# Kernel optimization log

Measured on AMD Instinct MI355X. Metric: run time of the kernel, lower is better.

## Reference

```python
import jax, jax.numpy as jnp
import numpy as np
from jax import lax

B, C, H, W = 4, 512, 32, 32
HEADS, HC, GROUPS = 8, 64, 4
GC = C // GROUPS          # group channels = 128
GH = HEADS // GROUPS      # heads per group = 2
KK = 5                    # offset conv kernel (stage_idx=2)
OFFSET_RANGE_FACTOR = 2.0
LN_EPS = 1e-5


def conv1x1(x, w, b):
    # x: [B,Cin,H,W], w: [Cout,Cin], b: [Cout]
    return jnp.einsum('bchw,oc->bohw', x, w) + b[None, :, None, None]


def ref_points(h, w, n, dtype=jnp.float32):
    # torch linspace(0.5, h-0.5, h) normalized to (-1,1); stacked (y,x)
    ry = ((jnp.arange(h, dtype=dtype) + 0.5) / h) * 2.0 - 1.0
    rx = ((jnp.arange(w, dtype=dtype) + 0.5) / w) * 2.0 - 1.0
    ref = jnp.stack(jnp.meshgrid(ry, rx, indexing='ij'), axis=-1)  # [h,w,2]
    return jnp.broadcast_to(ref[None], (n, h, w, 2))


def grid_sample(img, grid):
    # F.grid_sample: bilinear, align_corners=True, padding_mode='zeros'
    # img: [N,C,Hs,Ws], grid: [N,*S,2] with grid[...,0]=x, grid[...,1]=y in [-1,1]
    N, Cc, Hs, Ws = img.shape
    gx = (grid[..., 0] + 1.0) * 0.5 * (Ws - 1)
    gy = (grid[..., 1] + 1.0) * 0.5 * (Hs - 1)
    x0 = jnp.floor(gx)
    y0 = jnp.floor(gy)
    wx1 = gx - x0
    wy1 = gy - y0
    imgf = img.reshape(N, Cc, Hs * Ws)

    def corner(ix, iy, wgt):
        valid = ((ix >= 0) & (ix <= Ws - 1) & (iy >= 0) & (iy <= Hs - 1)).astype(img.dtype)
        flat = (jnp.clip(iy, 0, Hs - 1) * Ws + jnp.clip(ix, 0, Ws - 1)).astype(jnp.int32)
        vals = jax.vmap(lambda im, f: im[:, f])(imgf, flat)  # [N,C,*S]
        return vals * (wgt * valid)[:, None]

    return (corner(x0, y0, (1 - wx1) * (1 - wy1))
            + corner(x0 + 1, y0, wx1 * (1 - wy1))
            + corner(x0, y0 + 1, (1 - wx1) * wy1)
            + corner(x0 + 1, y0 + 1, wx1 * wy1))


def setup_inputs() -> dict:
    key = jax.random.key(0)
    ks = jax.random.split(key, 10)

    def w(k, shape, s=0.02):
        return jax.random.normal(k, shape, jnp.float32) * s

    return {
        'x': jax.random.normal(ks[0], (B, C, H, W), jnp.float32),
        'w_q': w(ks[1], (C, C)), 'b_q': jnp.zeros((C,), jnp.float32),
        'w_k': w(ks[2], (C, C)), 'b_k': jnp.zeros((C,), jnp.float32),
        'w_v': w(ks[3], (C, C)), 'b_v': jnp.zeros((C,), jnp.float32),
        'w_o': w(ks[4], (C, C)), 'b_o': jnp.zeros((C,), jnp.float32),
        'dw_w': w(ks[5], (GC, 1, KK, KK), 0.05),  # depthwise offset conv
        'dw_b': jnp.zeros((GC,), jnp.float32),
        'ln_g': jnp.ones((GC,), jnp.float32),
        'ln_b': jnp.zeros((GC,), jnp.float32),
        'off_w': w(ks[6], (2, GC), 0.05),          # 1x1 conv -> 2 offset channels
        'rpe': w(ks[7], (HEADS, 2 * H - 1, 2 * W - 1), 0.01),
    }


def reference(x, w_q, b_q, w_k, b_k, w_v, b_v, w_o, b_o,
              dw_w, dw_b, ln_g, ln_b, off_w, rpe):
    q = conv1x1(x, w_q, b_q)
    # 'b (g c) h w -> (b g) c h w'
    q_off = q.reshape(B * GROUPS, GC, H, W)
    # depthwise conv kk=5, stride=1, pad=2
    off = lax.conv_general_dilated(q_off, dw_w, (1, 1),
                                   ((KK // 2, KK // 2), (KK // 2, KK // 2)),
                                   dimension_numbers=('NCHW', 'OIHW', 'NCHW'),
                                   feature_group_count=GC) + dw_b[None, :, None, None]
    # LayerNormProxy over channel dim
    mu = jnp.mean(off, axis=1, keepdims=True)
    var = jnp.mean((off - mu) ** 2, axis=1, keepdims=True)
    off = (off - mu) * lax.rsqrt(var + LN_EPS) * ln_g[None, :, None, None] + ln_b[None, :, None, None]
    off = jax.nn.gelu(off, approximate=False)
    off = jnp.einsum('bchw,oc->bohw', off, off_w)  # [B*G, 2, Hk, Wk] (y,x channels)
    Hk, Wk = off.shape[2], off.shape[3]
    nS = Hk * Wk
    off_range = jnp.array([1.0 / Hk, 1.0 / Wk], dtype=x.dtype).reshape(1, 2, 1, 1)
    off = jnp.tanh(off) * off_range * OFFSET_RANGE_FACTOR
    off = jnp.transpose(off, (0, 2, 3, 1))  # [B*G, Hk, Wk, 2]
    ref = ref_points(Hk, Wk, B * GROUPS, x.dtype)
    pos = off + ref  # offset_range_factor >= 0 branch
    # deformable sampling (grid takes (x,y))
    xs = grid_sample(x.reshape(B * GROUPS, GC, H, W), pos[..., ::-1])  # [B*G,GC,Hk,Wk]
    xs = xs.reshape(B, C, 1, nS)
    qf = q.reshape(B * HEADS, HC, H * W)
    k = conv1x1(xs, w_k, b_k).reshape(B * HEADS, HC, nS)
    v = conv1x1(xs, w_v, b_v).reshape(B * HEADS, HC, nS)
    attn = jnp.einsum('bcm,bcn->bmn', qf, k) * (HC ** -0.5)  # [B*Hd, HW, nS]
    # continuous relative-position bias via bilinear table lookup
    rpe_b = jnp.broadcast_to(rpe[None], (B,) + rpe.shape).reshape(
        B * GROUPS, GH, rpe.shape[1], rpe.shape[2])
    q_grid = ref_points(H, W, B * GROUPS, x.dtype)
    disp = (q_grid.reshape(B * GROUPS, H * W, 1, 2)
            - pos.reshape(B * GROUPS, 1, nS, 2)) * 0.5  # [B*G, HW, nS, 2]
    bias = grid_sample(rpe_b, disp[..., ::-1]).reshape(B * HEADS, H * W, nS)
    attn = jax.nn.softmax(attn + bias, axis=2)
    out = jnp.einsum('bmn,bcn->bcm', attn, v).reshape(B, C, H, W)
    y = conv1x1(out, w_o, b_o)
    return (y,
            pos.reshape(B, GROUPS, Hk, Wk, 2),
            ref.reshape(B, GROUPS, Hk, Wk, 2))
```

## Files before the change

kernel.cpp:

```cpp
#include <hip/hip_runtime.h>
#include <hip/hip_bf16.h>

typedef __hip_bfloat16 bf16;
typedef __attribute__((ext_vector_type(8))) short bf16x8;
typedef __attribute__((ext_vector_type(4))) float f32x4;

#define BDIM 4
#define CDIM 512
#define NHEADS 8
#define NGROUPS 4
#define GCH 128

__device__ __forceinline__ float bf2f(bf16 v) { return __bfloat162float(v); }
__device__ __forceinline__ float bfu2f(unsigned short u) {
  return __uint_as_float(((unsigned)u) << 16);
}
__device__ __forceinline__ unsigned short f2bu(float v) {
  return __hip_bfloat16_raw(__float2bfloat16(v)).x;
}
__device__ __forceinline__ unsigned pack2(float lo, float hi) {
  return (unsigned)f2bu(lo) | ((unsigned)f2bu(hi) << 16);
}

template <bool IN_F32, typename OutT, int NMAT>
__global__ __launch_bounds__(256) void gemm_kernel(
    const float* __restrict__ W0, const float* __restrict__ bias0,
    const float* __restrict__ W1, const float* __restrict__ bias1,
    const void* __restrict__ in,
    OutT* __restrict__ out0, OutT* __restrict__ out1) {
  __shared__ __align__(16) unsigned char smem[8192 * (NMAT + 1)];
  unsigned char* b_lds = smem + 8192 * NMAT;
  const int b = blockIdx.z;
  const int o0 = blockIdx.y * 64;
  const int n0 = blockIdx.x * 64;
  const int t = threadIdx.x, l = t & 63, w = t >> 6;
  const int rg = l >> 4, cl = l & 15;
  const int o_base = (w >> 1) * 32, n_base = (w & 1) * 32;
  const int ao = t >> 2;
  const int ac8 = (t & 3) * 8;
  const int kc2 = (t & 31) * 2;
  const int kn8 = (t >> 5) * 8;
  const unsigned swo = (unsigned)((ao & 7) << 4);
  const float* Ws[2] = {W0, W1};
  const float* Bs[2] = {bias0, bias1};
  OutT* Os[2] = {out0, out1};

  f32x4 acc[NMAT][2][2];
#pragma unroll
  for (int m = 0; m < NMAT; m++)
#pragma unroll
    for (int i = 0; i < 2; i++)
#pragma unroll
      for (int j = 0; j < 2; j++) acc[m][i][j] = {0.f, 0.f, 0.f, 0.f};

  for (int k0 = 0; k0 < 512; k0 += 64) {
#pragma unroll
    for (int m = 0; m < NMAT; m++) {
      const float* wr = Ws[m] + (size_t)(o0 + ao) * 512 + k0;
      const float4 a0 = *(const float4*)(wr + ac8);
      const float4 a1 = *(const float4*)(wr + ac8 + 4);
      const float4 c0 = *(const float4*)(wr + ac8 + 32);
      const float4 c1 = *(const float4*)(wr + ac8 + 36);
      uint4 ua = {pack2(a0.x, a0.y), pack2(a0.z, a0.w),
                  pack2(a1.x, a1.y), pack2(a1.z, a1.w)};
      uint4 ub = {pack2(c0.x, c0.y), pack2(c0.z, c0.w),
                  pack2(c1.x, c1.y), pack2(c1.z, c1.w)};
      unsigned char* am = smem + 8192 * m;
      *(uint4*)(am + ao * 128 + ((2 * ac8) ^ swo)) = ua;
      *(uint4*)(am + ao * 128 + ((2 * ac8 + 64) ^ swo)) = ub;
    }
    if constexpr (IN_F32) {
      const float* inb = (const float*)in + (size_t)b * 524288;
      const float* p0 = inb + (size_t)(k0 + kc2) * 1024 + n0 + kn8;
      union { float4 v[2]; float f[8]; } r0, r1;
      r0.v[0] = *(const float4*)p0;
      r0.v[1] = *(const float4*)(p0 + 4);
      r1.v[0] = *(const float4*)(p0 + 1024);
      r1.v[1] = *(const float4*)(p0 + 1028);
#pragma unroll
      for (int i = 0; i < 8; i++) {
        const int n = kn8 + i;
        *(unsigned*)(b_lds + n * 128 + ((2 * kc2) ^ ((n & 7) << 4))) =
            pack2(r0.f[i], r1.f[i]);
      }
    } else {
      const unsigned short* inb = (const unsigned short*)in + (size_t)b * 524288;
      union { uint4 v; unsigned short hw[8]; } r0, r1;
      r0.v = *(const uint4*)(inb + (size_t)(k0 + kc2) * 1024 + n0 + kn8);
      r1.v = *(const uint4*)(inb + (size_t)(k0 + kc2 + 1) * 1024 + n0 + kn8);
#pragma unroll
      for (int i = 0; i < 8; i++) {
        const int n = kn8 + i;
        const unsigned v32 = (unsigned)r0.hw[i] | ((unsigned)r1.hw[i] << 16);
        *(unsigned*)(b_lds + n * 128 + ((2 * kc2) ^ ((n & 7) << 4))) = v32;
      }
    }
    __syncthreads();
#pragma unroll
    for (int kk = 0; kk < 2; kk++) {
      bf16x8 bfr[2];
#pragma unroll
      for (int nn = 0; nn < 2; nn++) {
        const int n_loc = n_base + 16 * nn + cl;
        bfr[nn] = *(const bf16x8*)(b_lds + n_loc * 128 +
                                   ((64 * kk + 16 * rg) ^ ((n_loc & 7) << 4)));
      }
#pragma unroll
      for (int m = 0; m < NMAT; m++) {
        bf16x8 af[2];
#pragma unroll
        for (int mi = 0; mi < 2; mi++) {
          const int o_loc = o_base + 16 * mi + cl;
          af[mi] = *(const bf16x8*)(smem + 8192 * m + o_loc * 128 +
                                    ((64 * kk + 16 * rg) ^ ((o_loc & 7) << 4)));
        }
#pragma unroll
        for (int mi = 0; mi < 2; mi++)
#pragma unroll
          for (int nn = 0; nn < 2; nn++)
            acc[m][mi][nn] = __builtin_amdgcn_mfma_f32_16x16x32_bf16(
                af[mi], bfr[nn], acc[m][mi][nn], 0, 0, 0);
      }
    }
    __syncthreads();
  }

  float* o_st = (float*)smem;
#pragma unroll
  for (int m = 0; m < NMAT; m++) {
    __syncthreads();
#pragma unroll
    for (int mi = 0; mi < 2; mi++)
#pragma unroll
      for (int nn = 0; nn < 2; nn++)
#pragma unroll
        for (int r = 0; r < 4; r++)
          o_st[(o_base + 16 * mi + 4 * rg + r) * 64 + n_base + 16 * nn + cl] =
              acc[m][mi][nn][r];
    __syncthreads();
    const int eo = t >> 4;
    const int en = (t & 15) * 4;
#pragma unroll
    for (int pass = 0; pass < 4; pass++) {
      const int o_loc = eo + pass * 16;
      const f32x4 v = *(const f32x4*)(o_st + o_loc * 64 + en);
      const float bv = Bs[m][o0 + o_loc];
      if constexpr (sizeof(OutT) == 2) {
        ushort4 u;
        u.x = f2bu(v[0] + bv);
        u.y = f2bu(v[1] + bv);
        u.z = f2bu(v[2] + bv);
        u.w = f2bu(v[3] + bv);
        *(ushort4*)((bf16*)Os[m] + ((size_t)b * 512 + o0 + o_loc) * 1024 + n0 + en) = u;
      } else {
        float4 r = {v[0] + bv, v[1] + bv, v[2] + bv, v[3] + bv};
        *(float4*)((float*)Os[m] + ((size_t)b * 512 + o0 + o_loc) * 1024 + n0 + en) = r;
      }
    }
  }
}

__global__ __launch_bounds__(512) void offset_kernel(
    const bf16* __restrict__ q, const float* __restrict__ dw_w,
    const float* __restrict__ dw_b, const float* __restrict__ ln_g,
    const float* __restrict__ ln_b, const float* __restrict__ off_w,
    float* __restrict__ pos, float* __restrict__ out_pos, float* __restrict__ out_ref) {
  __shared__ unsigned short q_s[5][36][128];
  __shared__ float red_a[4][2][2];
  __shared__ float red_p[4][2][2];
  const int bg = blockIdx.x;
  const int h = blockIdx.y;
  const int b = bg >> 2, g = bg & 3;
  const int t = threadIdx.x;

  for (int task = t; task < 640; task += 512) {
    const int ky = task >> 7, c = task & 127;
    const int y = h + ky - 2;
    if (y >= 0 && y < 32) {
      const unsigned short* qrow =
          (const unsigned short*)q + ((size_t)b * CDIM + g * GCH + c) * 1024 + y * 32;
      q_s[ky][0][c] = 0;
      q_s[ky][1][c] = 0;
#pragma unroll
      for (int x8 = 0; x8 < 4; x8++) {
        union { uint4 u; unsigned short s[8]; } vv;
        vv.u = *(const uint4*)(qrow + x8 * 8);
#pragma unroll
        for (int i = 0; i < 8; i++) q_s[ky][2 + x8 * 8 + i][c] = vv.s[i];
      }
      q_s[ky][34][c] = 0;
      q_s[ky][35][c] = 0;
    } else {
#pragma unroll
      for (int xi = 0; xi < 36; xi++) q_s[ky][xi][c] = 0;
    }
  }

  const int wslot = t >> 7;
  const int c = t & 127;
  const int half = c >> 6;
  const int lane = t & 63;
  float wgt[25];
#pragma unroll
  for (int i = 0; i < 25; i++) wgt[i] = dw_w[c * 25 + i];
  const float cbias = dw_b[c];
  const float gam = ln_g[c], bet = ln_b[c];
  const float ow0 = off_w[c], ow1 = off_w[GCH + c];
  __syncthreads();

  for (int j = 0; j < 8; j++) {
    const int w = wslot * 8 + j;
    float s = cbias;
#pragma unroll
    for (int ky = 0; ky < 5; ky++)
#pragma unroll
      for (int kx = 0; kx < 5; kx++)
        s += wgt[ky * 5 + kx] * bfu2f(q_s[ky][w + kx][c]);
    float ssum = s, ssq = s * s;
#pragma unroll
    for (int o = 1; o < 64; o <<= 1) {
      ssum += __shfl_xor(ssum, o);
      ssq += __shfl_xor(ssq, o);
    }
    if (lane == 0) { red_a[wslot][half][0] = ssum; red_a[wslot][half][1] = ssq; }
    __syncthreads();
    const float mu = (red_a[wslot][0][0] + red_a[wslot][1][0]) * (1.0f / 128.0f);
    const float var = (red_a[wslot][0][1] + red_a[wslot][1][1]) * (1.0f / 128.0f) - mu * mu;
    const float xn = (s - mu) * rsqrtf(var + 1e-5f) * gam + bet;
    const float ge = 0.5f * xn * (1.0f + erff(xn * 0.70710678118654752f));
    float p0 = ow0 * ge, p1 = ow1 * ge;
#pragma unroll
    for (int o = 1; o < 64; o <<= 1) {
      p0 += __shfl_xor(p0, o);
      p1 += __shfl_xor(p1, o);
    }
    if (lane == 0) { red_p[wslot][half][0] = p0; red_p[wslot][half][1] = p1; }
    __syncthreads();
    if (c == 0) {
      const float oy = tanhf(red_p[wslot][0][0] + red_p[wslot][1][0]) * 0.0625f;
      const float ox = tanhf(red_p[wslot][0][1] + red_p[wslot][1][1]) * 0.0625f;
      const float ry = ((float)h + 0.5f) * (2.0f / 32.0f) - 1.0f;
      const float rx = ((float)w + 0.5f) * (2.0f / 32.0f) - 1.0f;
      const float py = oy + ry, px = ox + rx;
      const size_t idx = (size_t)bg * 1024 + h * 32 + w;
      pos[idx * 2] = py;
      pos[idx * 2 + 1] = px;
      out_pos[idx * 2] = py;
      out_pos[idx * 2 + 1] = px;
      out_ref[idx * 2] = ry;
      out_ref[idx * 2 + 1] = rx;
    }
  }
}

__global__ __launch_bounds__(256) void sample_kernel(
    const float* __restrict__ x, const float* __restrict__ pos, bf16* __restrict__ xs) {
  const int bg = blockIdx.x, c = blockIdx.y;
  const int b = bg >> 2, g = bg & 3;
  __shared__ float plane[1024];
  const float* xp = x + ((size_t)b * CDIM + g * GCH + c) * 1024;
  for (int i = threadIdx.x; i < 1024; i += 256) plane[i] = xp[i];
  __syncthreads();
  for (int s = threadIdx.x; s < 1024; s += 256) {
    const float py = pos[((size_t)bg * 1024 + s) * 2];
    const float px = pos[((size_t)bg * 1024 + s) * 2 + 1];
    const float gx = (px + 1.0f) * 15.5f;
    const float gy = (py + 1.0f) * 15.5f;
    const float x0f = floorf(gx), y0f = floorf(gy);
    const float wx = gx - x0f, wy = gy - y0f;
    const int ix = (int)x0f, iy = (int)y0f;
    float r = 0.0f;
    const bool vx0 = (ix >= 0) & (ix <= 31), vx1 = (ix + 1 >= 0) & (ix + 1 <= 31);
    const bool vy0 = (iy >= 0) & (iy <= 31), vy1 = (iy + 1 >= 0) & (iy + 1 <= 31);
    if (vy0 && vx0) r += plane[iy * 32 + ix] * (1.0f - wx) * (1.0f - wy);
    if (vy0 && vx1) r += plane[iy * 32 + ix + 1] * wx * (1.0f - wy);
    if (vy1 && vx0) r += plane[(iy + 1) * 32 + ix] * (1.0f - wx) * wy;
    if (vy1 && vx1) r += plane[(iy + 1) * 32 + ix + 1] * wx * wy;
    xs[((size_t)bg * GCH + c) * 1024 + s] = __float2bfloat16(r);
  }
}

__global__ __launch_bounds__(512) void attn_kernel(
    const bf16* __restrict__ q, const bf16* __restrict__ kk,
    const bf16* __restrict__ vv, const float* __restrict__ pos,
    const float* __restrict__ rpe, bf16* __restrict__ ao) {
  __shared__ __align__(16) unsigned char smem[51976];
  float* rpe_f = (float*)(smem + 32768);
  float* m_x = (float*)(smem + 50952);
  float* s_x = (float*)(smem + 51464);

  const int bh = blockIdx.y;
  const int m0 = blockIdx.x * 64;
  const int b = bh >> 3, h = bh & 7;
  const int g = h >> 1;
  const int bg = b * 4 + g;
  const int t = threadIdx.x, l = t & 63, w = t >> 6;
  const int wq = w & 3, half = w >> 2;
  const int rg = l >> 4, cl = l & 15;
  const int t2 = t & 255;
  const size_t hbase = ((size_t)b * CDIM + h * 64) * 1024;
  const unsigned short* qu = (const unsigned short*)q;

  unsigned char* k_base = smem + half * 8192;
  unsigned char* v_base = smem + 16384 + half * 8192;
  float* pos_a = (float*)(smem + 49928) + half * 128;

  for (int i = t; i < 65 * 66; i += 512) {
    const int y = i / 66, x = i - y * 66;
    float v = 0.0f;
    if (y >= 1 && y <= 63 && x >= 1 && x <= 63)
      v = rpe[h * 3969 + (y - 1) * 63 + (x - 1)];
    rpe_f[i] = v;
  }

  const int qloc = 16 * wq + cl;
  const int qm = m0 + qloc;
  const float qy15 = 15.5f * (((float)(qm >> 5) + 0.5f) * (2.0f / 32.0f) - 1.0f);
  const float qx15 = 15.5f * (((float)(qm & 31) + 0.5f) * (2.0f / 32.0f) - 1.0f);

  bf16x8 bq[2];
#pragma unroll
  for (int kc = 0; kc < 2; kc++) {
    bf16x8 a;
#pragma unroll
    for (int j = 0; j < 8; j++)
      a[j] = (short)qu[hbase + (size_t)(32 * kc + 8 * rg + j) * 1024 + qm];
    bq[kc] = a;
  }

  float rmax = -1e30f, rsum = 0.0f;
  f32x4 oacc[4] = {{0.f,0.f,0.f,0.f},{0.f,0.f,0.f,0.f},
                   {0.f,0.f,0.f,0.f},{0.f,0.f,0.f,0.f}};

  const float* posb = pos + (size_t)bg * 2048;
  const unsigned swl = (unsigned)((cl & 7) << 4);
  const int kc2 = (t2 & 31) * 2;
  const int kn8 = (t2 >> 5) * 8;
  const int vc = t2 >> 2;
  const int vh = (t2 & 3) * 32;

  for (int tile = 0; tile < 8; tile++) {
    const int n0 = half * 512 + tile * 64;
    {
      union { uint4 v; unsigned short hw[8]; } r0, r1;
      r0.v = *(const uint4*)(kk + hbase + (size_t)kc2 * 1024 + n0 + kn8);
      r1.v = *(const uint4*)(kk + hbase + (size_t)(kc2 + 1) * 1024 + n0 + kn8);
#pragma unroll
      for (int i = 0; i < 8; i++) {
        const int n = kn8 + i;
        const unsigned v32 = (unsigned)r0.hw[i] | ((unsigned)r1.hw[i] << 16);
        *(unsigned*)(k_base + n * 128 + ((kc2 * 2) ^ ((n & 7) << 4))) = v32;
      }
      const uint4 s0 = *(const uint4*)(vv + hbase + (size_t)vc * 1024 + n0 + vh / 2);
      const uint4 s1 = *(const uint4*)(vv + hbase + (size_t)vc * 1024 + n0 + vh / 2 + 8);
      *(uint4*)(v_base + vc * 128 + (vh ^ ((vc & 7) << 4))) = s0;
      *(uint4*)(v_base + vc * 128 + ((vh + 16) ^ ((vc & 7) << 4))) = s1;
      if (t2 < 128) pos_a[t2] = 31.0f - 15.5f * posb[2 * n0 + t2];
    }
    __syncthreads();

    f32x4 sf[4];
#pragma unroll
    for (int tn = 0; tn < 4; tn++) {
      const int nrow = 16 * tn + cl;
      const bf16x8 a0 = *(const bf16x8*)(k_base + nrow * 128 + ((16 * rg) ^ swl));
      const bf16x8 a1 = *(const bf16x8*)(k_base + nrow * 128 + ((64 + 16 * rg) ^ swl));
      f32x4 z = {0.f, 0.f, 0.f, 0.f};
      z = __builtin_amdgcn_mfma_f32_16x16x32_bf16(a0, bq[0], z, 0, 0, 0);
      z = __builtin_amdgcn_mfma_f32_16x16x32_bf16(a1, bq[1], z, 0, 0, 0);
      sf[tn] = z;
    }

#pragma unroll
    for (int tn = 0; tn < 4; tn++)
#pragma unroll
      for (int r = 0; r < 4; r++) {
        const int key = 16 * tn + 4 * rg + r;
        const float gyc = qy15 + pos_a[2 * key];
        const float gxc = qx15 + pos_a[2 * key + 1];
        const float y0f = floorf(gyc), x0f = floorf(gxc);
        const float wy = gyc - y0f, wx = gxc - x0f;
        const int iy1 = (int)y0f + 1, ix1 = (int)x0f + 1;
        const float* tp = rpe_f + iy1 * 66 + ix1;
        const float t00 = tp[0], t01 = tp[1];
        const float t10 = tp[66], t11 = tp[67];
        const float r0v = t00 + (t01 - t00) * wx;
        const float r1v = t10 + (t11 - t10) * wx;
        const float bias = r0v + (r1v - r0v) * wy;
        sf[tn][r] = sf[tn][r] * 0.125f + bias;
      }

    float tmax = sf[0][0];
#pragma unroll
    for (int tn = 0; tn < 4; tn++)
#pragma unroll
      for (int r = 0; r < 4; r++) tmax = fmaxf(tmax, sf[tn][r]);
    tmax = fmaxf(tmax, __shfl_xor(tmax, 16));
    tmax = fmaxf(tmax, __shfl_xor(tmax, 32));
    const float nmax = fmaxf(rmax, tmax);
    const float corr = __expf(rmax - nmax);
    rmax = nmax;
    float lsum = 0.0f;
    unsigned pw[8];
#pragma unroll
    for (int tn = 0; tn < 4; tn++) {
      const float p0 = __expf(sf[tn][0] - nmax);
      const float p1 = __expf(sf[tn][1] - nmax);
      const float p2 = __expf(sf[tn][2] - nmax);
      const float p3 = __expf(sf[tn][3] - nmax);
      lsum += (p0 + p1) + (p2 + p3);
      pw[2 * tn] = pack2(p0, p1);
      pw[2 * tn + 1] = pack2(p2, p3);
    }
    lsum += __shfl_xor(lsum, 16);
    lsum += __shfl_xor(lsum, 32);
    rsum = rsum * corr + lsum;
#pragma unroll
    for (int tc = 0; tc < 4; tc++) {
      oacc[tc][0] *= corr; oacc[tc][1] *= corr;
      oacc[tc][2] *= corr; oacc[tc][3] *= corr;
    }

    __syncthreads();

#pragma unroll
    for (int tn = 0; tn < 4; tn++) {
      *(unsigned*)(k_base + qloc * 128 + ((2 * (16 * tn + 4 * rg)) ^ swl)) = pw[2 * tn];
      *(unsigned*)(k_base + qloc * 128 + ((2 * (16 * tn + 4 * rg) + 4) ^ swl)) = pw[2 * tn + 1];
    }

#pragma unroll
    for (int kc = 0; kc < 2; kc++) {
      const bf16x8 pb = *(const bf16x8*)(k_base + qloc * 128 + ((2 * (32 * kc + 8 * rg)) ^ swl));
#pragma unroll
      for (int tc = 0; tc < 4; tc++) {
        const int crow = 16 * tc + cl;
        const bf16x8 av = *(const bf16x8*)(v_base + crow * 128 + ((2 * (32 * kc + 8 * rg)) ^ swl));
        oacc[tc] = __builtin_amdgcn_mfma_f32_16x16x32_bf16(av, pb, oacc[tc], 0, 0, 0);
      }
    }
    __syncthreads();
  }

  if (l < 16) {
    m_x[half * 64 + wq * 16 + cl] = rmax;
    s_x[half * 64 + wq * 16 + cl] = rsum;
  }
  __syncthreads();
  const float m0v = m_x[wq * 16 + cl], m1v = m_x[64 + wq * 16 + cl];
  const float s0v = s_x[wq * 16 + cl], s1v = s_x[64 + wq * 16 + cl];
  const float M = fmaxf(m0v, m1v);
  const float f0 = __expf(m0v - M), f1 = __expf(m1v - M);
  const float inv = 1.0f / (f0 * s0v + f1 * s1v);
  const float scale = (half == 0 ? f0 : f1) * inv;
  float* o_st = (float*)smem;
  if (half == 0) {
#pragma unroll
    for (int tc = 0; tc < 4; tc++)
#pragma unroll
      for (int r = 0; r < 4; r++)
        o_st[(16 * tc + 4 * rg + r) * 66 + qloc] = oacc[tc][r] * scale;
  }
  __syncthreads();
  if (half == 1) {
#pragma unroll
    for (int tc = 0; tc < 4; tc++)
#pragma unroll
      for (int r = 0; r < 4; r++)
        o_st[(16 * tc + 4 * rg + r) * 66 + qloc] += oacc[tc][r] * scale;
  }
  __syncthreads();
  {
    const int c = t >> 3, mq = (t & 7) * 8;
    unsigned u[4];
#pragma unroll
    for (int i = 0; i < 4; i++)
      u[i] = pack2(o_st[c * 66 + mq + 2 * i], o_st[c * 66 + mq + 2 * i + 1]);
    uint4 outv = {u[0], u[1], u[2], u[3]};
    *(uint4*)(ao + hbase + (size_t)c * 1024 + m0 + mq) = outv;
  }
}

extern "C" void kernel_launch(void* const* d_in, const int* in_sizes, int n_in,
                              void* d_out, int out_size, void* d_ws, size_t ws_size,
                              hipStream_t stream) {
  const float* x    = (const float*)d_in[0];
  const float* w_q  = (const float*)d_in[1];
  const float* b_q  = (const float*)d_in[2];
  const float* w_k  = (const float*)d_in[3];
  const float* b_k  = (const float*)d_in[4];
  const float* w_v  = (const float*)d_in[5];
  const float* b_v  = (const float*)d_in[6];
  const float* w_o  = (const float*)d_in[7];
  const float* b_o  = (const float*)d_in[8];
  const float* dw_w = (const float*)d_in[9];
  const float* dw_b = (const float*)d_in[10];
  const float* ln_g = (const float*)d_in[11];
  const float* ln_b = (const float*)d_in[12];
  const float* off_w= (const float*)d_in[13];
  const float* rpe  = (const float*)d_in[14];

  float* out_y   = (float*)d_out;
  float* out_pos = out_y + 2097152;
  float* out_ref = out_pos + 32768;

  float* pos_ws = (float*)d_ws;
  bf16*  q_ws   = (bf16*)(pos_ws + 32768);
  bf16*  xs_ws  = q_ws + 2097152;
  bf16*  k_ws   = xs_ws + 2097152;
  bf16*  v_ws   = k_ws + 2097152;
  bf16*  ao_ws  = xs_ws;

  gemm_kernel<true, bf16, 1><<<dim3(16, 8, 4), 256, 0, stream>>>(
      w_q, b_q, nullptr, nullptr, x, q_ws, (bf16*)nullptr);
  offset_kernel<<<dim3(16, 32), 512, 0, stream>>>(q_ws, dw_w, dw_b, ln_g, ln_b, off_w,
                                                  pos_ws, out_pos, out_ref);
  sample_kernel<<<dim3(16, 128), 256, 0, stream>>>(x, pos_ws, xs_ws);
  gemm_kernel<false, bf16, 2><<<dim3(16, 8, 4), 256, 0, stream>>>(
      w_k, b_k, w_v, b_v, xs_ws, k_ws, v_ws);
  attn_kernel<<<dim3(16, 32), 512, 0, stream>>>(q_ws, k_ws, v_ws, pos_ws, rpe, ao_ws);
  gemm_kernel<false, float, 1><<<dim3(16, 8, 4), 256, 0, stream>>>(
      w_o, b_o, nullptr, nullptr, ao_ws, out_y, (float*)nullptr);
}
```

Baseline: 112.6 us.

## Split attention key range across four wave groups with 1024-thread blocks

The attention kernel now uses 1024 threads per block and splits the key dimension four ways instead of two. Each quarter processes 4 tiles of 64 keys instead of 8. The four partial softmax states are merged through shared memory, with two partial output buffers summed at the store. The RPE bias table is stored in shared memory as bf16 rather than fp32 so that the doubled K/V staging still fits. This aims to shorten the serial loop per block and raise wave count on the 512-block grid, at the cost of more shared memory, more merge work, and slightly lower precision in the bias.

```diff
diff --git a/kernel.cpp b/kernel.cpp
--- a/kernel.cpp
+++ b/kernel.cpp
@@ -280,14 +280,14 @@
   }
 }
 
-__global__ __launch_bounds__(512) void attn_kernel(
+__global__ __launch_bounds__(1024, 8) void attn_kernel(
     const bf16* __restrict__ q, const bf16* __restrict__ kk,
     const bf16* __restrict__ vv, const float* __restrict__ pos,
     const float* __restrict__ rpe, bf16* __restrict__ ao) {
-  __shared__ __align__(16) unsigned char smem[51976];
-  float* rpe_f = (float*)(smem + 32768);
-  float* m_x = (float*)(smem + 50952);
-  float* s_x = (float*)(smem + 51464);
+  __shared__ __align__(16) unsigned char smem[78216];
+  unsigned short* rpe_s = (unsigned short*)(smem + 65536);
+  float* m_x = (float*)(smem + 76168);
+  float* s_x = (float*)(smem + 77192);
 
   const int bh = blockIdx.y;
   const int m0 = blockIdx.x * 64;
@@ -295,22 +295,22 @@
   const int g = h >> 1;
   const int bg = b * 4 + g;
   const int t = threadIdx.x, l = t & 63, w = t >> 6;
-  const int wq = w & 3, half = w >> 2;
+  const int wq = w & 3, quarter = w >> 2;
   const int rg = l >> 4, cl = l & 15;
   const int t2 = t & 255;
   const size_t hbase = ((size_t)b * CDIM + h * 64) * 1024;
   const unsigned short* qu = (const unsigned short*)q;
 
-  unsigned char* k_base = smem + half * 8192;
-  unsigned char* v_base = smem + 16384 + half * 8192;
-  float* pos_a = (float*)(smem + 49928) + half * 128;
-
-  for (int i = t; i < 65 * 66; i += 512) {
+  unsigned char* k_base = smem + quarter * 8192;
+  unsigned char* v_base = smem + 32768 + quarter * 8192;
+  float* pos_a = (float*)(smem + 74120) + quarter * 128;
+
+  for (int i = t; i < 65 * 66; i += 1024) {
     const int y = i / 66, x = i - y * 66;
-    float v = 0.0f;
+    unsigned short v = 0;
     if (y >= 1 && y <= 63 && x >= 1 && x <= 63)
-      v = rpe[h * 3969 + (y - 1) * 63 + (x - 1)];
-    rpe_f[i] = v;
+      v = f2bu(rpe[h * 3969 + (y - 1) * 63 + (x - 1)]);
+    rpe_s[i] = v;
   }
 
   const int qloc = 16 * wq + cl;
@@ -339,8 +339,8 @@
   const int vc = t2 >> 2;
   const int vh = (t2 & 3) * 32;
 
-  for (int tile = 0; tile < 8; tile++) {
-    const int n0 = half * 512 + tile * 64;
+  for (int tile = 0; tile < 4; tile++) {
+    const int n0 = quarter * 256 + tile * 64;
     {
       union { uint4 v; unsigned short hw[8]; } r0, r1;
       r0.v = *(const uint4*)(kk + hbase + (size_t)kc2 * 1024 + n0 + kn8);
@@ -381,9 +381,9 @@
         const float y0f = floorf(gyc), x0f = floorf(gxc);
         const float wy = gyc - y0f, wx = gxc - x0f;
         const int iy1 = (int)y0f + 1, ix1 = (int)x0f + 1;
-        const float* tp = rpe_f + iy1 * 66 + ix1;
-        const float t00 = tp[0], t01 = tp[1];
-        const float t10 = tp[66], t11 = tp[67];
+        const unsigned short* tp = rpe_s + iy1 * 66 + ix1;
+        const float t00 = bfu2f(tp[0]), t01 = bfu2f(tp[1]);
+        const float t10 = bfu2f(tp[66]), t11 = bfu2f(tp[67]);
         const float r0v = t00 + (t01 - t00) * wx;
         const float r1v = t10 + (t11 - t10) * wx;
         const float bias = r0v + (r1v - r0v) * wy;
@@ -443,41 +443,50 @@
   }
 
   if (l < 16) {
-    m_x[half * 64 + wq * 16 + cl] = rmax;
-    s_x[half * 64 + wq * 16 + cl] = rsum;
+    m_x[quarter * 64 + qloc] = rmax;
+    s_x[quarter * 64 + qloc] = rsum;
   }
   __syncthreads();
-  const float m0v = m_x[wq * 16 + cl], m1v = m_x[64 + wq * 16 + cl];
-  const float s0v = s_x[wq * 16 + cl], s1v = s_x[64 + wq * 16 + cl];
-  const float M = fmaxf(m0v, m1v);
-  const float f0 = __expf(m0v - M), f1 = __expf(m1v - M);
-  const float inv = 1.0f / (f0 * s0v + f1 * s1v);
-  const float scale = (half == 0 ? f0 : f1) * inv;
-  float* o_st = (float*)smem;
-  if (half == 0) {
+  float mq4[4], sq4[4];
+#pragma unroll
+  for (int qq = 0; qq < 4; qq++) {
+    mq4[qq] = m_x[qq * 64 + qloc];
+    sq4[qq] = s_x[qq * 64 + qloc];
+  }
+  const float M = fmaxf(fmaxf(mq4[0], mq4[1]), fmaxf(mq4[2], mq4[3]));
+  const float e0 = __expf(mq4[0] - M), e1 = __expf(mq4[1] - M);
+  const float e2 = __expf(mq4[2] - M), e3 = __expf(mq4[3] - M);
+  const float inv = 1.0f / (e0 * sq4[0] + e1 * sq4[1] + e2 * sq4[2] + e3 * sq4[3]);
+  const float eq[4] = {e0, e1, e2, e3};
+  const float scale = eq[quarter] * inv;
+  float* o_stA = (float*)smem;
+  float* o_stB = (float*)(smem + 20480);
+  float* mine = (quarter & 1) ? o_stB : o_stA;
+  if (quarter < 2) {
 #pragma unroll
     for (int tc = 0; tc < 4; tc++)
 #pragma unroll
       for (int r = 0; r < 4; r++)
-        o_st[(16 * tc + 4 * rg + r) * 66 + qloc] = oacc[tc][r] * scale;
+        mine[(16 * tc + 4 * rg + r) * 66 + qloc] = oacc[tc][r] * scale;
   }
   __syncthreads();
-  if (half == 1) {
+  if (quarter >= 2) {
 #pragma unroll
     for (int tc = 0; tc < 4; tc++)
 #pragma unroll
       for (int r = 0; r < 4; r++)
-        o_st[(16 * tc + 4 * rg + r) * 66 + qloc] += oacc[tc][r] * scale;
+        mine[(16 * tc + 4 * rg + r) * 66 + qloc] += oacc[tc][r] * scale;
   }
   __syncthreads();
   {
-    const int c = t >> 3, mq = (t & 7) * 8;
-    unsigned u[4];
-#pragma unroll
-    for (int i = 0; i < 4; i++)
-      u[i] = pack2(o_st[c * 66 + mq + 2 * i], o_st[c * 66 + mq + 2 * i + 1]);
-    uint4 outv = {u[0], u[1], u[2], u[3]};
-    *(uint4*)(ao + hbase + (size_t)c * 1024 + m0 + mq) = outv;
+    const int c = t >> 4, mq = (t & 15) * 4;
+    const int base = c * 66 + mq;
+    const float v0 = o_stA[base] + o_stB[base];
+    const float v1 = o_stA[base + 1] + o_stB[base + 1];
+    const float v2 = o_stA[base + 2] + o_stB[base + 2];
+    const float v3 = o_stA[base + 3] + o_stB[base + 3];
+    uint2 outv = {pack2(v0, v1), pack2(v2, v3)};
+    *(uint2*)(ao + hbase + (size_t)c * 1024 + m0 + mq) = outv;
   }
 }
 
@@ -518,7 +527,7 @@
   sample_kernel<<<dim3(16, 128), 256, 0, stream>>>(x, pos_ws, xs_ws);
   gemm_kernel<false, bf16, 2><<<dim3(16, 8, 4), 256, 0, stream>>>(
       w_k, b_k, w_v, b_v, xs_ws, k_ws, v_ws);
-  attn_kernel<<<dim3(16, 32), 512, 0, stream>>>(q_ws, k_ws, v_ws, pos_ws, rpe, ao_ws);
+  attn_kernel<<<dim3(16, 32), 1024, 0, stream>>>(q_ws, k_ws, v_ws, pos_ws, rpe, ao_ws);
   gemm_kernel<false, float, 1><<<dim3(16, 8, 4), 256, 0, stream>>>(
       w_o, b_o, nullptr, nullptr, ao_ws, out_y, (float*)nullptr);
 }
```

Result: slower. 244.6 us (+117.3%).

## Split attention keys across two blocks with a separate combine kernel

Applied to the files above, without the earlier changes.

Adds a grid z dimension so each attention block handles half the keys, raising the grid from 512 to 1024 blocks on a 256-CU device. Each block writes unnormalized partial outputs plus its max and sum to workspace, and a new combine kernel merges the two halves into bf16. The RPE table in shared memory is also stored as bf16, shrinking LDS use so more blocks may fit per CU. In exchange it adds fp32 partial traffic, an extra kernel launch, and slightly lower bias precision.

```diff
diff --git a/kernel.cpp b/kernel.cpp
--- a/kernel.cpp
+++ b/kernel.cpp
@@ -283,14 +283,16 @@
 __global__ __launch_bounds__(512) void attn_kernel(
     const bf16* __restrict__ q, const bf16* __restrict__ kk,
     const bf16* __restrict__ vv, const float* __restrict__ pos,
-    const float* __restrict__ rpe, bf16* __restrict__ ao) {
-  __shared__ __align__(16) unsigned char smem[51976];
-  float* rpe_f = (float*)(smem + 32768);
-  float* m_x = (float*)(smem + 50952);
-  float* s_x = (float*)(smem + 51464);
+    const float* __restrict__ rpe, float* __restrict__ Op,
+    float* __restrict__ Mp, float* __restrict__ Sp) {
+  __shared__ __align__(16) unsigned char smem[43400];
+  unsigned short* rpe_s = (unsigned short*)(smem + 32768);
+  float* m_x = (float*)(smem + 42372);
+  float* s_x = (float*)(smem + 42884);
 
   const int bh = blockIdx.y;
   const int m0 = blockIdx.x * 64;
+  const int z = blockIdx.z;
   const int b = bh >> 3, h = bh & 7;
   const int g = h >> 1;
   const int bg = b * 4 + g;
@@ -303,14 +305,14 @@
 
   unsigned char* k_base = smem + half * 8192;
   unsigned char* v_base = smem + 16384 + half * 8192;
-  float* pos_a = (float*)(smem + 49928) + half * 128;
+  float* pos_a = (float*)(smem + 41348) + half * 128;
 
   for (int i = t; i < 65 * 66; i += 512) {
     const int y = i / 66, x = i - y * 66;
-    float v = 0.0f;
+    unsigned short v = 0;
     if (y >= 1 && y <= 63 && x >= 1 && x <= 63)
-      v = rpe[h * 3969 + (y - 1) * 63 + (x - 1)];
-    rpe_f[i] = v;
+      v = f2bu(rpe[h * 3969 + (y - 1) * 63 + (x - 1)]);
+    rpe_s[i] = v;
   }
 
   const int qloc = 16 * wq + cl;
@@ -339,8 +341,8 @@
   const int vc = t2 >> 2;
   const int vh = (t2 & 3) * 32;
 
-  for (int tile = 0; tile < 8; tile++) {
-    const int n0 = half * 512 + tile * 64;
+  for (int tile = 0; tile < 4; tile++) {
+    const int n0 = z * 512 + half * 256 + tile * 64;
     {
       union { uint4 v; unsigned short hw[8]; } r0, r1;
       r0.v = *(const uint4*)(kk + hbase + (size_t)kc2 * 1024 + n0 + kn8);
@@ -365,10 +367,10 @@
       const int nrow = 16 * tn + cl;
       const bf16x8 a0 = *(const bf16x8*)(k_base + nrow * 128 + ((16 * rg) ^ swl));
       const bf16x8 a1 = *(const bf16x8*)(k_base + nrow * 128 + ((64 + 16 * rg) ^ swl));
-      f32x4 z = {0.f, 0.f, 0.f, 0.f};
-      z = __builtin_amdgcn_mfma_f32_16x16x32_bf16(a0, bq[0], z, 0, 0, 0);
-      z = __builtin_amdgcn_mfma_f32_16x16x32_bf16(a1, bq[1], z, 0, 0, 0);
-      sf[tn] = z;
+      f32x4 zz = {0.f, 0.f, 0.f, 0.f};
+      zz = __builtin_amdgcn_mfma_f32_16x16x32_bf16(a0, bq[0], zz, 0, 0, 0);
+      zz = __builtin_amdgcn_mfma_f32_16x16x32_bf16(a1, bq[1], zz, 0, 0, 0);
+      sf[tn] = zz;
     }
 
 #pragma unroll
@@ -381,9 +383,9 @@
         const float y0f = floorf(gyc), x0f = floorf(gxc);
         const float wy = gyc - y0f, wx = gxc - x0f;
         const int iy1 = (int)y0f + 1, ix1 = (int)x0f + 1;
-        const float* tp = rpe_f + iy1 * 66 + ix1;
-        const float t00 = tp[0], t01 = tp[1];
-        const float t10 = tp[66], t11 = tp[67];
+        const unsigned short* tp = rpe_s + iy1 * 66 + ix1;
+        const float t00 = bfu2f(tp[0]), t01 = bfu2f(tp[1]);
+        const float t10 = bfu2f(tp[66]), t11 = bfu2f(tp[67]);
         const float r0v = t00 + (t01 - t00) * wx;
         const float r1v = t10 + (t11 - t10) * wx;
         const float bias = r0v + (r1v - r0v) * wy;
@@ -443,23 +445,27 @@
   }
 
   if (l < 16) {
-    m_x[half * 64 + wq * 16 + cl] = rmax;
-    s_x[half * 64 + wq * 16 + cl] = rsum;
+    m_x[half * 64 + qloc] = rmax;
+    s_x[half * 64 + qloc] = rsum;
   }
   __syncthreads();
-  const float m0v = m_x[wq * 16 + cl], m1v = m_x[64 + wq * 16 + cl];
-  const float s0v = s_x[wq * 16 + cl], s1v = s_x[64 + wq * 16 + cl];
+  const float m0v = m_x[qloc], m1v = m_x[64 + qloc];
+  const float s0v = s_x[qloc], s1v = s_x[64 + qloc];
   const float M = fmaxf(m0v, m1v);
   const float f0 = __expf(m0v - M), f1 = __expf(m1v - M);
-  const float inv = 1.0f / (f0 * s0v + f1 * s1v);
-  const float scale = (half == 0 ? f0 : f1) * inv;
+  const float scale = (half == 0 ? f0 : f1);
   float* o_st = (float*)smem;
+  const int pidx = (z * 32 + bh) * 16 + blockIdx.x;
   if (half == 0) {
 #pragma unroll
     for (int tc = 0; tc < 4; tc++)
 #pragma unroll
       for (int r = 0; r < 4; r++)
-        o_st[(16 * tc + 4 * rg + r) * 66 + qloc] = oacc[tc][r] * scale;
+        o_st[(16 * tc + 4 * rg + r) * 68 + qloc] = oacc[tc][r] * scale;
+    if (l < 16) {
+      Mp[pidx * 64 + qloc] = M;
+      Sp[pidx * 64 + qloc] = f0 * s0v + f1 * s1v;
+    }
   }
   __syncthreads();
   if (half == 1) {
@@ -467,17 +473,50 @@
     for (int tc = 0; tc < 4; tc++)
 #pragma unroll
       for (int r = 0; r < 4; r++)
-        o_st[(16 * tc + 4 * rg + r) * 66 + qloc] += oacc[tc][r] * scale;
+        o_st[(16 * tc + 4 * rg + r) * 68 + qloc] += oacc[tc][r] * scale;
   }
   __syncthreads();
   {
-    const int c = t >> 3, mq = (t & 7) * 8;
-    unsigned u[4];
-#pragma unroll
-    for (int i = 0; i < 4; i++)
-      u[i] = pack2(o_st[c * 66 + mq + 2 * i], o_st[c * 66 + mq + 2 * i + 1]);
-    uint4 outv = {u[0], u[1], u[2], u[3]};
-    *(uint4*)(ao + hbase + (size_t)c * 1024 + m0 + mq) = outv;
+    const int c = t >> 3, q8 = (t & 7) * 8;
+    const float4 v0 = *(const float4*)(o_st + c * 68 + q8);
+    const float4 v1 = *(const float4*)(o_st + c * 68 + q8 + 4);
+    float* dst = Op + (size_t)pidx * 4096 + c * 64 + q8;
+    *(float4*)dst = v0;
+    *(float4*)(dst + 4) = v1;
+  }
+}
+
+__global__ __launch_bounds__(256) void combine_kernel(
+    const float* __restrict__ Op, const float* __restrict__ Mp,
+    const float* __restrict__ Sp, bf16* __restrict__ ao) {
+  const int mt = blockIdx.x, bh = blockIdx.y;
+  const int b = bh >> 3, h = bh & 7;
+  __shared__ float sc0[64], sc1[64];
+  const int t = threadIdx.x;
+  const int i0 = (bh * 16 + mt) * 64;
+  const int i1 = ((32 + bh) * 16 + mt) * 64;
+  if (t < 64) {
+    const float m0 = Mp[i0 + t], m1 = Mp[i1 + t];
+    const float s0 = Sp[i0 + t], s1 = Sp[i1 + t];
+    const float M = fmaxf(m0, m1);
+    const float e0 = __expf(m0 - M), e1 = __expf(m1 - M);
+    const float inv = 1.0f / (e0 * s0 + e1 * s1);
+    sc0[t] = e0 * inv;
+    sc1[t] = e1 * inv;
+  }
+  __syncthreads();
+  const size_t ob0 = (size_t)(bh * 16 + mt) * 4096;
+  const size_t ob1 = (size_t)((32 + bh) * 16 + mt) * 4096;
+  const size_t hbase = ((size_t)b * CDIM + h * 64) * 1024;
+  for (int i = t * 4; i < 4096; i += 1024) {
+    const int c = i >> 6, qq = i & 63;
+    const float4 a = *(const float4*)(Op + ob0 + i);
+    const float4 b4 = *(const float4*)(Op + ob1 + i);
+    const float4 s0v = *(const float4*)&sc0[qq];
+    const float4 s1v = *(const float4*)&sc1[qq];
+    uint2 o = {pack2(a.x * s0v.x + b4.x * s1v.x, a.y * s0v.y + b4.y * s1v.y),
+               pack2(a.z * s0v.z + b4.z * s1v.z, a.w * s0v.w + b4.w * s1v.w)};
+    *(uint2*)(ao + hbase + (size_t)c * 1024 + mt * 64 + qq) = o;
   }
 }
 
@@ -509,6 +548,9 @@
   bf16*  xs_ws  = q_ws + 2097152;
   bf16*  k_ws   = xs_ws + 2097152;
   bf16*  v_ws   = k_ws + 2097152;
+  float* Op_ws  = (float*)(v_ws + 2097152);
+  float* Mp_ws  = Op_ws + 4194304;
+  float* Sp_ws  = Mp_ws + 65536;
   bf16*  ao_ws  = xs_ws;
 
   gemm_kernel<true, bf16, 1><<<dim3(16, 8, 4), 256, 0, stream>>>(
@@ -518,7 +560,9 @@
   sample_kernel<<<dim3(16, 128), 256, 0, stream>>>(x, pos_ws, xs_ws);
   gemm_kernel<false, bf16, 2><<<dim3(16, 8, 4), 256, 0, stream>>>(
       w_k, b_k, w_v, b_v, xs_ws, k_ws, v_ws);
-  attn_kernel<<<dim3(16, 32), 512, 0, stream>>>(q_ws, k_ws, v_ws, pos_ws, rpe, ao_ws);
+  attn_kernel<<<dim3(16, 32, 2), 512, 0, stream>>>(q_ws, k_ws, v_ws, pos_ws, rpe,
+                                                   Op_ws, Mp_ws, Sp_ws);
+  combine_kernel<<<dim3(16, 32), 256, 0, stream>>>(Op_ws, Mp_ws, Sp_ws, ao_ws);
   gemm_kernel<false, float, 1><<<dim3(16, 8, 4), 256, 0, stream>>>(
       w_o, b_o, nullptr, nullptr, ao_ws, out_y, (float*)nullptr);
 }
```

New measurement: 216.0 us. 1.92x slower.

## Prefetch next K/V tile into registers, give P its own buffer, store RPE as bf16

Applied to the files above, without the earlier changes.

The attention kernel now issues the global loads for the next K/V/pos tile right after the barrier, so they overlap with the current tile's MFMA and softmax work. P gets a dedicated LDS region, which removes one __syncthreads per tile. The RPE bias table is kept in LDS as bf16 instead of fp32 to make room for that region, and s_setprio raises wave priority around the MFMA sections. In exchange the kernel uses more registers and more LDS (about 58KB), which may lower occupancy, and the bias values lose precision.

```diff
diff --git a/kernel.cpp b/kernel.cpp
--- a/kernel.cpp
+++ b/kernel.cpp
@@ -284,10 +284,10 @@
     const bf16* __restrict__ q, const bf16* __restrict__ kk,
     const bf16* __restrict__ vv, const float* __restrict__ pos,
     const float* __restrict__ rpe, bf16* __restrict__ ao) {
-  __shared__ __align__(16) unsigned char smem[51976];
-  float* rpe_f = (float*)(smem + 32768);
-  float* m_x = (float*)(smem + 50952);
-  float* s_x = (float*)(smem + 51464);
+  __shared__ __align__(16) unsigned char smem[59784];
+  unsigned short* rpe_s = (unsigned short*)(smem + 49152);
+  float* m_x = (float*)(smem + 58756);
+  float* s_x = (float*)(smem + 59268);
 
   const int bh = blockIdx.y;
   const int m0 = blockIdx.x * 64;
@@ -303,14 +303,15 @@
 
   unsigned char* k_base = smem + half * 8192;
   unsigned char* v_base = smem + 16384 + half * 8192;
-  float* pos_a = (float*)(smem + 49928) + half * 128;
+  unsigned char* p_base = smem + 32768 + half * 8192;
+  float* pos_a = (float*)(smem + 57732) + half * 128;
 
   for (int i = t; i < 65 * 66; i += 512) {
     const int y = i / 66, x = i - y * 66;
-    float v = 0.0f;
+    unsigned short v = 0;
     if (y >= 1 && y <= 63 && x >= 1 && x <= 63)
-      v = rpe[h * 3969 + (y - 1) * 63 + (x - 1)];
-    rpe_f[i] = v;
+      v = f2bu(rpe[h * 3969 + (y - 1) * 63 + (x - 1)]);
+    rpe_s[i] = v;
   }
 
   const int qloc = 16 * wq + cl;
@@ -339,27 +340,39 @@
   const int vc = t2 >> 2;
   const int vh = (t2 & 3) * 32;
 
+  uint4 kr0, kr1, vr0, vr1;
+  float pr = 0.0f;
+  auto issue_load = [&](int tile) {
+    const int n0 = half * 512 + tile * 64;
+    kr0 = *(const uint4*)(kk + hbase + (size_t)kc2 * 1024 + n0 + kn8);
+    kr1 = *(const uint4*)(kk + hbase + (size_t)(kc2 + 1) * 1024 + n0 + kn8);
+    vr0 = *(const uint4*)(vv + hbase + (size_t)vc * 1024 + n0 + vh / 2);
+    vr1 = *(const uint4*)(vv + hbase + (size_t)vc * 1024 + n0 + vh / 2 + 8);
+    if (t2 < 128) pr = posb[2 * n0 + t2];
+  };
+
+  issue_load(0);
   for (int tile = 0; tile < 8; tile++) {
-    const int n0 = half * 512 + tile * 64;
     {
       union { uint4 v; unsigned short hw[8]; } r0, r1;
-      r0.v = *(const uint4*)(kk + hbase + (size_t)kc2 * 1024 + n0 + kn8);
-      r1.v = *(const uint4*)(kk + hbase + (size_t)(kc2 + 1) * 1024 + n0 + kn8);
+      r0.v = kr0;
+      r1.v = kr1;
 #pragma unroll
       for (int i = 0; i < 8; i++) {
         const int n = kn8 + i;
         const unsigned v32 = (unsigned)r0.hw[i] | ((unsigned)r1.hw[i] << 16);
         *(unsigned*)(k_base + n * 128 + ((kc2 * 2) ^ ((n & 7) << 4))) = v32;
       }
-      const uint4 s0 = *(const uint4*)(vv + hbase + (size_t)vc * 1024 + n0 + vh / 2);
-      const uint4 s1 = *(const uint4*)(vv + hbase + (size_t)vc * 1024 + n0 + vh / 2 + 8);
-      *(uint4*)(v_base + vc * 128 + (vh ^ ((vc & 7) << 4))) = s0;
-      *(uint4*)(v_base + vc * 128 + ((vh + 16) ^ ((vc & 7) << 4))) = s1;
-      if (t2 < 128) pos_a[t2] = 31.0f - 15.5f * posb[2 * n0 + t2];
-    }
-    __syncthreads();
+      *(uint4*)(v_base + vc * 128 + (vh ^ ((vc & 7) << 4))) = vr0;
+      *(uint4*)(v_base + vc * 128 + ((vh + 16) ^ ((vc & 7) << 4))) = vr1;
+      if (t2 < 128) pos_a[t2] = 31.0f - 15.5f * pr;
+    }
+    __syncthreads();
+
+    if (tile < 7) issue_load(tile + 1);
 
     f32x4 sf[4];
+    __builtin_amdgcn_s_setprio(1);
 #pragma unroll
     for (int tn = 0; tn < 4; tn++) {
       const int nrow = 16 * tn + cl;
@@ -370,6 +383,7 @@
       z = __builtin_amdgcn_mfma_f32_16x16x32_bf16(a1, bq[1], z, 0, 0, 0);
       sf[tn] = z;
     }
+    __builtin_amdgcn_s_setprio(0);
 
 #pragma unroll
     for (int tn = 0; tn < 4; tn++)
@@ -381,9 +395,9 @@
         const float y0f = floorf(gyc), x0f = floorf(gxc);
         const float wy = gyc - y0f, wx = gxc - x0f;
         const int iy1 = (int)y0f + 1, ix1 = (int)x0f + 1;
-        const float* tp = rpe_f + iy1 * 66 + ix1;
-        const float t00 = tp[0], t01 = tp[1];
-        const float t10 = tp[66], t11 = tp[67];
+        const unsigned short* tp = rpe_s + iy1 * 66 + ix1;
+        const float t00 = bfu2f(tp[0]), t01 = bfu2f(tp[1]);
+        const float t10 = bfu2f(tp[66]), t11 = bfu2f(tp[67]);
         const float r0v = t00 + (t01 - t00) * wx;
         const float r1v = t10 + (t11 - t10) * wx;
         const float bias = r0v + (r1v - r0v) * wy;
@@ -421,17 +435,16 @@
       oacc[tc][2] *= corr; oacc[tc][3] *= corr;
     }
 
-    __syncthreads();
-
 #pragma unroll
     for (int tn = 0; tn < 4; tn++) {
-      *(unsigned*)(k_base + qloc * 128 + ((2 * (16 * tn + 4 * rg)) ^ swl)) = pw[2 * tn];
-      *(unsigned*)(k_base + qloc * 128 + ((2 * (16 * tn + 4 * rg) + 4) ^ swl)) = pw[2 * tn + 1];
-    }
-
+      *(unsigned*)(p_base + qloc * 128 + ((2 * (16 * tn + 4 * rg)) ^ swl)) = pw[2 * tn];
+      *(unsigned*)(p_base + qloc * 128 + ((2 * (16 * tn + 4 * rg) + 4) ^ swl)) = pw[2 * tn + 1];
+    }
+
+    __builtin_amdgcn_s_setprio(1);
 #pragma unroll
     for (int kc = 0; kc < 2; kc++) {
-      const bf16x8 pb = *(const bf16x8*)(k_base + qloc * 128 + ((2 * (32 * kc + 8 * rg)) ^ swl));
+      const bf16x8 pb = *(const bf16x8*)(p_base + qloc * 128 + ((2 * (32 * kc + 8 * rg)) ^ swl));
 #pragma unroll
       for (int tc = 0; tc < 4; tc++) {
         const int crow = 16 * tc + cl;
@@ -439,16 +452,17 @@
         oacc[tc] = __builtin_amdgcn_mfma_f32_16x16x32_bf16(av, pb, oacc[tc], 0, 0, 0);
       }
     }
+    __builtin_amdgcn_s_setprio(0);
     __syncthreads();
   }
 
   if (l < 16) {
-    m_x[half * 64 + wq * 16 + cl] = rmax;
-    s_x[half * 64 + wq * 16 + cl] = rsum;
+    m_x[half * 64 + qloc] = rmax;
+    s_x[half * 64 + qloc] = rsum;
   }
   __syncthreads();
-  const float m0v = m_x[wq * 16 + cl], m1v = m_x[64 + wq * 16 + cl];
-  const float s0v = s_x[wq * 16 + cl], s1v = s_x[64 + wq * 16 + cl];
+  const float m0v = m_x[qloc], m1v = m_x[64 + qloc];
+  const float s0v = s_x[qloc], s1v = s_x[64 + qloc];
   const float M = fmaxf(m0v, m1v);
   const float f0 = __expf(m0v - M), f1 = __expf(m1v - M);
   const float inv = 1.0f / (f0 * s0v + f1 * s1v);
```

Result: slower. 213.2 us (+89.3%).
